# Kernel tuning notes

Measured on AMD Instinct MI355X. Metric: run time of the kernel, lower is better.

Reference implementation:

```python
import jax, jax.numpy as jnp
import numpy as np

B, H, W, C = 4, 256, 256, 256
WS = 8          # window size (both dims)
HEADS = 1
SEQ = WS * WS   # 64 tokens per window
NW = B * (H // WS) * (W // WS)  # 4096 windows
INNER = C * HEADS


def setup_inputs() -> dict:
    key = jax.random.key(0)
    k1, k2, k3, k4 = jax.random.split(key, 4)
    x = jax.random.normal(k1, (B, H, W, C), dtype=jnp.float32)
    attn = jax.random.uniform(k2, (NW, HEADS, SEQ, SEQ), dtype=jnp.float32)
    # to_v: Linear(dim, inner_dim, bias=False); stored as [in, out] for x @ Wv
    Wv = jax.random.normal(k3, (C, INNER), dtype=jnp.float32) * (C ** -0.5)
    # to_out: Linear(inner_dim, dim)
    Wo = jax.random.normal(k4, (INNER, C), dtype=jnp.float32) * (INNER ** -0.5)
    bo = jnp.zeros((C,), dtype=jnp.float32)
    return {"x": x, "attn": attn, "Wv": Wv, "Wo": Wo, "bo": bo}


def reference(x, attn, Wv, Wo, bo):
    b, h, w, c = x.shape
    nh, nw = h // WS, w // WS
    # window partition: b (h b0) (w b1) c -> (b h w) (b0 b1) c
    xw = x.reshape(b, nh, WS, nw, WS, c).transpose(0, 1, 3, 2, 4, 5)
    xw = xw.reshape(b * nh * nw, SEQ, c)
    # value projection, split heads: n s (h d) -> n h s d
    v = (xw @ Wv).reshape(-1, SEQ, HEADS, c).transpose(0, 2, 1, 3)
    # precomputed-attention weighted sum
    out = jnp.einsum('nhij,nhjd->nhid', attn, v)
    # merge heads: n h s d -> n s (h d)
    out = out.transpose(0, 2, 1, 3).reshape(-1, SEQ, HEADS * c)
    out = out @ Wo + bo
    # window un-partition: (b h w) (b0 b1) c -> b (h b0) (w b1) c
    out = out.reshape(b, nh, nw, WS, WS, c).transpose(0, 1, 3, 2, 4, 5)
    return out.reshape(b, h, w, c)
```

## Files before the change

### kernel.cpp

```cpp
#include <hip/hip_runtime.h>
#include <hip/hip_bf16.h>


typedef __bf16 bf16x8 __attribute__((ext_vector_type(8)));
typedef __bf16 bf16x4 __attribute__((ext_vector_type(4)));
typedef float  f32x16 __attribute__((ext_vector_type(16)));
typedef float  f32x4  __attribute__((ext_vector_type(4)));

#define MFMA32(a, b, c) __builtin_amdgcn_mfma_f32_32x32x16_bf16(a, b, c, 0, 0, 0)

__global__ void wfuse_kernel(const float* __restrict__ Wv,
                             const float* __restrict__ Wo,
                             __bf16* __restrict__ WT) {
  const int n = blockIdx.x;
  const int k = threadIdx.x;
  const float* wvrow = Wv + k * 256;
  float acc = 0.f;
#pragma unroll 4
  for (int j = 0; j < 256; j += 4) {
    f32x4 wv = *(const f32x4*)(wvrow + j);
    acc += wv.x * Wo[(j + 0) * 256 + n];
    acc += wv.y * Wo[(j + 1) * 256 + n];
    acc += wv.z * Wo[(j + 2) * 256 + n];
    acc += wv.w * Wo[(j + 3) * 256 + n];
  }
  WT[n * 256 + k] = (__bf16)acc;
}

__global__ __launch_bounds__(256, 3)
void na_msa_kernel(const float* __restrict__ x,
                   const float* __restrict__ attn,
                   const __bf16* __restrict__ WT,
                   const float* __restrict__ bo,
                   float* __restrict__ out) {
  __shared__ char lds[40960];
  char* lds_xw = lds;
  char* lds_at = lds + 32768;

  const int t    = threadIdx.x;
  const int lane = t & 63;
  const int wv   = t >> 6;
  const int ln31 = lane & 31;
  const int lh   = lane >> 5;

  const int n  = blockIdx.x;
  const int wi = n & 31;
  const int hi = (n >> 5) & 31;
  const int b  = n >> 10;
  const long base = (((long)(b * 256 + hi * 8)) * 256 + wi * 8) * 256;
  const float* xp = x + base;

#pragma unroll
  for (int i = 0; i < 16; ++i) {
    int gi = i * 256 + t;
    int rowblk = gi >> 9;
    int f = gi & 511;
    f32x4 v = *(const f32x4*)(xp + rowblk * 65536 + f * 4);
    int tok = rowblk * 8 + (f >> 6);
    int ch0 = (f & 63) * 4;
    bf16x4 hv = { (__bf16)v.x, (__bf16)v.y, (__bf16)v.z, (__bf16)v.w };
    int byt = tok * 512 + ((ch0 * 2) ^ ((tok & 31) << 4));
    *(bf16x4*)(lds_xw + byt) = hv;
  }

  const float* ap = attn + (long)n * 4096;
#pragma unroll
  for (int i = 0; i < 4; ++i) {
    int fi = i * 256 + t;
    f32x4 v = *(const f32x4*)(ap + fi * 4);
    int row = fi >> 4;
    int k0 = (fi & 15) * 4;
    bf16x4 hv = { (__bf16)v.x, (__bf16)v.y, (__bf16)v.z, (__bf16)v.w };
    int byt = row * 128 + ((k0 * 2) ^ ((row & 7) << 4));
    *(bf16x4*)(lds_at + byt) = hv;
  }
  __syncthreads();

  f32x16 acc00 = {}, acc10 = {}, acc01 = {}, acc11 = {};
  const __bf16* wtp = WT + (wv * 64 + ln31) * 256 + 8 * lh;
#pragma unroll
  for (int ks = 0; ks < 16; ++ks) {
    int kk = ks * 16 + 8 * lh;
    int byt0 = ln31 * 512 + ((kk * 2) ^ (ln31 << 4));
    bf16x8 a0 = *(const bf16x8*)(lds_xw + byt0);
    bf16x8 a1 = *(const bf16x8*)(lds_xw + byt0 + 16384);
    bf16x8 b0 = *(const bf16x8*)(wtp + ks * 16);
    bf16x8 b1 = *(const bf16x8*)(wtp + 8192 + ks * 16);
    acc00 = MFMA32(a0, b0, acc00);
    acc10 = MFMA32(a1, b0, acc10);
    acc01 = MFMA32(a0, b1, acc01);
    acc11 = MFMA32(a1, b1, acc11);
  }
  __syncthreads();

  char* ztw = lds + (wv << 13);
#define ZWRITE(ACC, MT, NTL) do {                                         \
    int chl = (NTL) * 32 + ln31;                                          \
    int rb = chl * 128;                                                   \
    int sw = (chl & 7) << 4;                                              \
    _Pragma("unroll")                                                     \
    for (int g = 0; g < 4; ++g) {                                         \
      int tok0 = (MT) * 32 + g * 8 + 4 * lh;                              \
      bf16x4 hv = { (__bf16)ACC[4 * g + 0], (__bf16)ACC[4 * g + 1],       \
                    (__bf16)ACC[4 * g + 2], (__bf16)ACC[4 * g + 3] };     \
      *(bf16x4*)(ztw + rb + ((tok0 * 2) ^ sw)) = hv;                      \
    } } while (0)
  ZWRITE(acc00, 0, 0); ZWRITE(acc01, 0, 1);
  ZWRITE(acc10, 1, 0); ZWRITE(acc11, 1, 1);

  f32x16 o00 = {}, o10 = {}, o01 = {}, o11 = {};
#pragma unroll
  for (int ks = 0; ks < 4; ++ks) {
    int kk = ks * 16 + 8 * lh;
    int ab0 = ln31 * 128 + ((kk * 2) ^ ((ln31 & 7) << 4));
    bf16x8 a0 = *(const bf16x8*)(lds_at + ab0);
    bf16x8 a1 = *(const bf16x8*)(lds_at + ab0 + 4096);
    bf16x8 b0 = *(const bf16x8*)(ztw + ab0);
    bf16x8 b1 = *(const bf16x8*)(ztw + ab0 + 4096);
    o00 = MFMA32(a0, b0, o00);
    o10 = MFMA32(a1, b0, o10);
    o01 = MFMA32(a0, b1, o01);
    o11 = MFMA32(a1, b1, o11);
  }

  float* op = out + base;
  float bv0 = bo[wv * 64 + ln31];
  float bv1 = bo[wv * 64 + 32 + ln31];
#define OWRITE(ACC, MT, NTL) do {                                         \
    int ch = wv * 64 + (NTL) * 32 + ln31;                                 \
    float bv = (NTL) ? bv1 : bv0;                                         \
    _Pragma("unroll")                                                     \
    for (int r = 0; r < 16; ++r) {                                        \
      int tok = (MT) * 32 + (r & 3) + 8 * (r >> 2) + 4 * lh;              \
      op[(tok >> 3) * 65536 + (tok & 7) * 256 + ch] = ACC[r] + bv;        \
    } } while (0)
  OWRITE(o00, 0, 0); OWRITE(o01, 0, 1);
  OWRITE(o10, 1, 0); OWRITE(o11, 1, 1);
}

extern "C" void kernel_launch(void* const* d_in, const int* in_sizes, int n_in,
                              void* d_out, int out_size, void* d_ws, size_t ws_size,
                              hipStream_t stream) {
  const float* x    = (const float*)d_in[0];
  const float* attn = (const float*)d_in[1];
  const float* Wv   = (const float*)d_in[2];
  const float* Wo   = (const float*)d_in[3];
  const float* bo   = (const float*)d_in[4];
  float* out = (float*)d_out;
  __bf16* WT = (__bf16*)d_ws;

  wfuse_kernel<<<256, 256, 0, stream>>>(Wv, Wo, WT);
  na_msa_kernel<<<4096, 256, 0, stream>>>(x, attn, WT, bo, out);
}
```

Before: 188.2 us.

## Split window tile across eight waves with 32 channels each

Launches 512-thread blocks where each of eight waves computes 32 output channels instead of 64, halving per-wave accumulators and loader iterations. This aims to raise waves in flight to better hide global memory latency in a bandwidth-bound kernel. The trade-off is less register reuse of LDS A-fragments per MFMA and more LDS read traffic.

```diff
diff --git a/kernel.cpp b/kernel.cpp
--- a/kernel.cpp
+++ b/kernel.cpp
@@ -27,7 +27,7 @@
   WT[n * 256 + k] = (__bf16)acc;
 }
 
-__global__ __launch_bounds__(256, 3)
+__global__ __launch_bounds__(512, 8)
 void na_msa_kernel(const float* __restrict__ x,
                    const float* __restrict__ attn,
                    const __bf16* __restrict__ WT,
@@ -51,8 +51,8 @@
   const float* xp = x + base;
 
 #pragma unroll
-  for (int i = 0; i < 16; ++i) {
-    int gi = i * 256 + t;
+  for (int i = 0; i < 8; ++i) {
+    int gi = i * 512 + t;
     int rowblk = gi >> 9;
     int f = gi & 511;
     f32x4 v = *(const f32x4*)(xp + rowblk * 65536 + f * 4);
@@ -65,8 +65,8 @@
 
   const float* ap = attn + (long)n * 4096;
 #pragma unroll
-  for (int i = 0; i < 4; ++i) {
-    int fi = i * 256 + t;
+  for (int i = 0; i < 2; ++i) {
+    int fi = i * 512 + t;
     f32x4 v = *(const f32x4*)(ap + fi * 4);
     int row = fi >> 4;
     int k0 = (fi & 15) * 4;
@@ -76,8 +76,8 @@
   }
   __syncthreads();
 
-  f32x16 acc00 = {}, acc10 = {}, acc01 = {}, acc11 = {};
-  const __bf16* wtp = WT + (wv * 64 + ln31) * 256 + 8 * lh;
+  f32x16 acc0 = {}, acc1 = {};
+  const __bf16* wtp = WT + (wv * 32 + ln31) * 256 + 8 * lh;
 #pragma unroll
   for (int ks = 0; ks < 16; ++ks) {
     int kk = ks * 16 + 8 * lh;
@@ -85,30 +85,29 @@
     bf16x8 a0 = *(const bf16x8*)(lds_xw + byt0);
     bf16x8 a1 = *(const bf16x8*)(lds_xw + byt0 + 16384);
     bf16x8 b0 = *(const bf16x8*)(wtp + ks * 16);
-    bf16x8 b1 = *(const bf16x8*)(wtp + 8192 + ks * 16);
-    acc00 = MFMA32(a0, b0, acc00);
-    acc10 = MFMA32(a1, b0, acc10);
-    acc01 = MFMA32(a0, b1, acc01);
-    acc11 = MFMA32(a1, b1, acc11);
+    acc0 = MFMA32(a0, b0, acc0);
+    acc1 = MFMA32(a1, b0, acc1);
   }
   __syncthreads();
 
-  char* ztw = lds + (wv << 13);
-#define ZWRITE(ACC, MT, NTL) do {                                         \
-    int chl = (NTL) * 32 + ln31;                                          \
-    int rb = chl * 128;                                                   \
-    int sw = (chl & 7) << 4;                                              \
-    _Pragma("unroll")                                                     \
-    for (int g = 0; g < 4; ++g) {                                         \
-      int tok0 = (MT) * 32 + g * 8 + 4 * lh;                              \
-      bf16x4 hv = { (__bf16)ACC[4 * g + 0], (__bf16)ACC[4 * g + 1],       \
-                    (__bf16)ACC[4 * g + 2], (__bf16)ACC[4 * g + 3] };     \
-      *(bf16x4*)(ztw + rb + ((tok0 * 2) ^ sw)) = hv;                      \
-    } } while (0)
-  ZWRITE(acc00, 0, 0); ZWRITE(acc01, 0, 1);
-  ZWRITE(acc10, 1, 0); ZWRITE(acc11, 1, 1);
+  char* ztw = lds + (wv << 12);
+  {
+    int rb = ln31 * 128;
+    int sw = (ln31 & 7) << 4;
+#pragma unroll
+    for (int g = 0; g < 4; ++g) {
+      int tok0 = g * 8 + 4 * lh;
+      bf16x4 h0 = { (__bf16)acc0[4 * g + 0], (__bf16)acc0[4 * g + 1],
+                    (__bf16)acc0[4 * g + 2], (__bf16)acc0[4 * g + 3] };
+      *(bf16x4*)(ztw + rb + ((tok0 * 2) ^ sw)) = h0;
+      int tok1 = 32 + g * 8 + 4 * lh;
+      bf16x4 h1 = { (__bf16)acc1[4 * g + 0], (__bf16)acc1[4 * g + 1],
+                    (__bf16)acc1[4 * g + 2], (__bf16)acc1[4 * g + 3] };
+      *(bf16x4*)(ztw + rb + ((tok1 * 2) ^ sw)) = h1;
+    }
+  }
 
-  f32x16 o00 = {}, o10 = {}, o01 = {}, o11 = {};
+  f32x16 o0 = {}, o1 = {};
 #pragma unroll
   for (int ks = 0; ks < 4; ++ks) {
     int kk = ks * 16 + 8 * lh;
@@ -116,26 +115,23 @@
     bf16x8 a0 = *(const bf16x8*)(lds_at + ab0);
     bf16x8 a1 = *(const bf16x8*)(lds_at + ab0 + 4096);
     bf16x8 b0 = *(const bf16x8*)(ztw + ab0);
-    bf16x8 b1 = *(const bf16x8*)(ztw + ab0 + 4096);
-    o00 = MFMA32(a0, b0, o00);
-    o10 = MFMA32(a1, b0, o10);
-    o01 = MFMA32(a0, b1, o01);
-    o11 = MFMA32(a1, b1, o11);
+    o0 = MFMA32(a0, b0, o0);
+    o1 = MFMA32(a1, b0, o1);
   }
 
   float* op = out + base;
-  float bv0 = bo[wv * 64 + ln31];
-  float bv1 = bo[wv * 64 + 32 + ln31];
-#define OWRITE(ACC, MT, NTL) do {                                         \
-    int ch = wv * 64 + (NTL) * 32 + ln31;                                 \
-    float bv = (NTL) ? bv1 : bv0;                                         \
-    _Pragma("unroll")                                                     \
-    for (int r = 0; r < 16; ++r) {                                        \
-      int tok = (MT) * 32 + (r & 3) + 8 * (r >> 2) + 4 * lh;              \
-      op[(tok >> 3) * 65536 + (tok & 7) * 256 + ch] = ACC[r] + bv;        \
-    } } while (0)
-  OWRITE(o00, 0, 0); OWRITE(o01, 0, 1);
-  OWRITE(o10, 1, 0); OWRITE(o11, 1, 1);
+  const int ch = wv * 32 + ln31;
+  const float bv = bo[ch];
+#pragma unroll
+  for (int r = 0; r < 16; ++r) {
+    int tok = (r & 3) + 8 * (r >> 2) + 4 * lh;
+    op[(tok >> 3) * 65536 + (tok & 7) * 256 + ch] = o0[r] + bv;
+  }
+#pragma unroll
+  for (int r = 0; r < 16; ++r) {
+    int tok = 32 + (r & 3) + 8 * (r >> 2) + 4 * lh;
+    op[(tok >> 3) * 65536 + (tok & 7) * 256 + ch] = o1[r] + bv;
+  }
 }
 
 extern "C" void kernel_launch(void* const* d_in, const int* in_sizes, int n_in,
@@ -150,5 +146,5 @@
   __bf16* WT = (__bf16*)d_ws;
 
   wfuse_kernel<<<256, 256, 0, stream>>>(Wv, Wo, WT);
-  na_msa_kernel<<<4096, 256, 0, stream>>>(x, attn, WT, bo, out);
+  na_msa_kernel<<<4096, 512, 0, stream>>>(x, attn, WT, bo, out);
 }
```

New measurement: 176.4 us. 6.3% less time.
